# Performance work log

Measured on AMD Instinct MI355X. Metric: run time of the kernel, lower is better.

## Reference

```python
import jax, jax.numpy as jnp
import numpy as np

NK, NQ, D = 8192, 8192, 64


def setup_inputs() -> dict:
    key = jax.random.key(0)
    k1, k2, k3, k4 = jax.random.split(key, 4)
    K = jax.random.normal(k1, (NK, D), dtype=jnp.float32)
    V = jax.random.normal(k2, (NK, D), dtype=jnp.float32)
    Q = jax.random.normal(k3, (NQ, D), dtype=jnp.float32)
    m = jax.random.normal(k4, (NQ, NK), dtype=jnp.float32)  # additive edge/mask data
    return {"K": K, "V": V, "Q": Q, "m": m}


def reference(K, V, Q, m):
    d = Q.shape[-1]
    scale = 1.0 / jnp.sqrt(jnp.asarray(d, dtype=Q.dtype))
    # affinity: scaled dot product + additive m (edge information / mask)
    QKt = jnp.einsum("qd,kd->qk", Q, K) * scale + m  # [NQ, NK]
    # norm: softmax over keys
    QKt_n = jax.nn.softmax(QKt, axis=-1)
    return QKt_n @ V  # [NQ, D]
```

## Files before the change

### kernel.cpp

```cpp
#include <hip/hip_runtime.h>

#define NKK 8192
#define NQQ 8192
#define DDIM 64

typedef __attribute__((ext_vector_type(8))) short short8;
typedef __attribute__((ext_vector_type(4))) float f32x4;

static __device__ __forceinline__ unsigned short f2b(float x) {
  unsigned int u = __builtin_bit_cast(unsigned int, x);
  unsigned int r = (u + 0x7fffu + ((u >> 16) & 1u)) >> 16;
  return (unsigned short)r;
}

__global__ __launch_bounds__(256) void prep_kernel(
    const float* __restrict__ K, const float* __restrict__ V, const float* __restrict__ Q,
    unsigned short* __restrict__ Kb, unsigned short* __restrict__ Qb, unsigned short* __restrict__ Vtb) {
  __shared__ unsigned short vt[64][72];
  const int b = blockIdx.x, t = threadIdx.x;
  const size_t base = (size_t)b * 4096;
#pragma unroll
  for (int i = 0; i < 4; ++i) {
    size_t idx = base + (size_t)i * 1024 + (size_t)t * 4;
    float4 kv = *(const float4*)(K + idx);
    float4 qv = *(const float4*)(Q + idx);
    ushort4 ko, qo;
    ko.x = f2b(kv.x); ko.y = f2b(kv.y); ko.z = f2b(kv.z); ko.w = f2b(kv.w);
    qo.x = f2b(qv.x); qo.y = f2b(qv.y); qo.z = f2b(qv.z); qo.w = f2b(qv.w);
    *(ushort4*)(Kb + idx) = ko;
    *(ushort4*)(Qb + idx) = qo;
  }
  const int r0 = b * 64;
#pragma unroll
  for (int i = 0; i < 4; ++i) {
    int kl = (t >> 4) + i * 16;
    int c4 = (t & 15) * 4;
    float4 v = *(const float4*)(V + (size_t)(r0 + kl) * 64 + c4);
    vt[c4 + 0][kl] = f2b(v.x);
    vt[c4 + 1][kl] = f2b(v.y);
    vt[c4 + 2][kl] = f2b(v.z);
    vt[c4 + 3][kl] = f2b(v.w);
  }
  __syncthreads();
  {
    int d = t >> 2, kc = (t & 3) * 16;
    uint4 a0 = *(const uint4*)(&vt[d][kc]);
    uint4 a1 = *(const uint4*)(&vt[d][kc + 8]);
    *(uint4*)(Vtb + (size_t)d * NKK + r0 + kc) = a0;
    *(uint4*)(Vtb + (size_t)d * NKK + r0 + kc + 8) = a1;
  }
}

__global__ __launch_bounds__(512, 2) void attn_kernel(
    const float* __restrict__ mg, const unsigned short* __restrict__ Kb,
    const unsigned short* __restrict__ Qb, const unsigned short* __restrict__ Vtb,
    float* __restrict__ out) {
  __shared__ unsigned short Pl[8][32 * 40];
  __shared__ float accslot[4][8][4][64];
  __shared__ float lslot[4][8][4];

  const int tid = threadIdx.x;
  const int wid = tid >> 6;
  const int lane = tid & 63;
  const int c = lane & 15;
  const int g = lane >> 4;
  const int q0 = blockIdx.x * 32;

  const float LOG2E = 1.4426950408889634f;
  const float C1 = 0.125f * LOG2E;
  const float MM = -8.0f * LOG2E;

  short8 qf[4];
#pragma unroll
  for (int qs = 0; qs < 2; ++qs)
#pragma unroll
    for (int dh = 0; dh < 2; ++dh)
      qf[qs * 2 + dh] = __builtin_bit_cast(
          short8, *(const uint4*)(Qb + (size_t)(q0 + qs * 16 + c) * 64 + dh * 32 + 8 * g));

  f32x4 acc[2][4];
#pragma unroll
  for (int a = 0; a < 2; ++a)
#pragma unroll
    for (int b2 = 0; b2 < 4; ++b2) acc[a][b2] = f32x4{0.f, 0.f, 0.f, 0.f};
  float lsum[8];
#pragma unroll
  for (int n = 0; n < 8; ++n) lsum[n] = 0.f;

  unsigned short* Pw = &Pl[wid][0];
  const unsigned short* Pr = &Pl[wid][c * 40 + 8 * g];
  const unsigned int mbase = (unsigned int)(q0 + 4 * g) * (unsigned int)NKK + (unsigned int)c;

  float mA[16], mB[16];
  short8 kA[4], kB[4], vA[4], vB[4];

  auto loadM = [&](int t, float (&mb)[16]) {
    const unsigned int toff = (unsigned int)((wid + 8 * t) * 32);
    const float* mp = mg + mbase + toff;
#pragma unroll
    for (int qs = 0; qs < 2; ++qs)
#pragma unroll
      for (int ks = 0; ks < 2; ++ks)
#pragma unroll
        for (int i = 0; i < 4; ++i)
          mb[qs * 8 + ks * 4 + i] = mp[(unsigned int)(qs * 16 + i) * NKK + ks * 16];
  };

  auto loadKV = [&](int t, short8 (&kf)[4], short8 (&vf)[4]) {
    const int k0 = (wid + 8 * t) * 32;
#pragma unroll
    for (int ks = 0; ks < 2; ++ks)
#pragma unroll
      for (int dh = 0; dh < 2; ++dh)
        kf[ks * 2 + dh] = __builtin_bit_cast(
            short8, *(const uint4*)(Kb + (size_t)(k0 + ks * 16 + c) * 64 + dh * 32 + 8 * g));
#pragma unroll
    for (int dt = 0; dt < 4; ++dt)
      vf[dt] = __builtin_bit_cast(
          short8, *(const uint4*)(Vtb + (size_t)(dt * 16 + c) * NKK + k0 + 8 * g));
  };

  auto compute = [&](const float (&mb)[16], const short8 (&kf)[4], const short8 (&vf)[4]) {
    f32x4 s[2][2];
#pragma unroll
    for (int qs = 0; qs < 2; ++qs)
#pragma unroll
      for (int ks = 0; ks < 2; ++ks) {
        f32x4 z = f32x4{0.f, 0.f, 0.f, 0.f};
        z = __builtin_amdgcn_mfma_f32_16x16x32_bf16(qf[qs * 2 + 0], kf[ks * 2 + 0], z, 0, 0, 0);
        z = __builtin_amdgcn_mfma_f32_16x16x32_bf16(qf[qs * 2 + 1], kf[ks * 2 + 1], z, 0, 0, 0);
        s[qs][ks] = z;
      }
#pragma unroll
    for (int qs = 0; qs < 2; ++qs)
#pragma unroll
      for (int ks = 0; ks < 2; ++ks)
#pragma unroll
        for (int i = 0; i < 4; ++i) {
          float e = __builtin_fmaf(s[qs][ks][i], C1,
                                   __builtin_fmaf(mb[qs * 8 + ks * 4 + i], LOG2E, MM));
          float p = __builtin_amdgcn_exp2f(e);
          lsum[qs * 4 + i] += p;
          Pw[(qs * 16 + 4 * g + i) * 40 + ks * 16 + c] = f2b(p);
        }
    short8 pa[2];
#pragma unroll
    for (int qs = 0; qs < 2; ++qs)
      pa[qs] = __builtin_bit_cast(short8, *(const uint4*)(Pr + qs * 640));
#pragma unroll
    for (int qs = 0; qs < 2; ++qs)
#pragma unroll
      for (int dt = 0; dt < 4; ++dt)
        acc[qs][dt] = __builtin_amdgcn_mfma_f32_16x16x32_bf16(pa[qs], vf[dt], acc[qs][dt], 0, 0, 0);
  };

  loadM(0, mA);
  loadKV(0, kA, vA);
  for (int t = 0; t < 32; t += 2) {
    loadM(t + 1, mB);
    loadKV(t + 1, kB, vB);
    compute(mA, kA, vA);
    if (t + 2 < 32) {
      loadM(t + 2, mA);
      loadKV(t + 2, kA, vA);
    }
    compute(mB, kB, vB);
  }

#pragma unroll
  for (int n = 0; n < 8; ++n) {
    float v = lsum[n];
    v += __shfl_xor(v, 1);
    v += __shfl_xor(v, 2);
    v += __shfl_xor(v, 4);
    v += __shfl_xor(v, 8);
    lsum[n] = v;
  }

  auto writeSlot = [&](int slot) {
#pragma unroll
    for (int qs = 0; qs < 2; ++qs)
#pragma unroll
      for (int dt = 0; dt < 4; ++dt)
#pragma unroll
        for (int i = 0; i < 4; ++i) accslot[slot][qs * 4 + dt][i][lane] = acc[qs][dt][i];
    if (c == 0) {
#pragma unroll
      for (int n = 0; n < 8; ++n) lslot[slot][n][g] = lsum[n];
    }
  };
  auto addSlot = [&](int slot) {
#pragma unroll
    for (int qs = 0; qs < 2; ++qs)
#pragma unroll
      for (int dt = 0; dt < 4; ++dt)
#pragma unroll
        for (int i = 0; i < 4; ++i) acc[qs][dt][i] += accslot[slot][qs * 4 + dt][i][lane];
#pragma unroll
    for (int n = 0; n < 8; ++n) lsum[n] += lslot[slot][n][g];
  };

  if (wid >= 4) writeSlot(wid - 4);
  __syncthreads();
  if (wid < 4) addSlot(wid);
  __syncthreads();
  if (wid == 2 || wid == 3) writeSlot(wid - 2);
  __syncthreads();
  if (wid < 2) addSlot(wid);
  __syncthreads();
  if (wid == 1) writeSlot(0);
  __syncthreads();
  if (wid == 0) {
    addSlot(0);
#pragma unroll
    for (int qs = 0; qs < 2; ++qs)
#pragma unroll
      for (int i = 0; i < 4; ++i) {
        float rl = 1.0f / lsum[qs * 4 + i];
        int q = q0 + qs * 16 + 4 * g + i;
#pragma unroll
        for (int dt = 0; dt < 4; ++dt)
          out[(size_t)q * 64 + dt * 16 + c] = acc[qs][dt][i] * rl;
      }
  }
}

extern "C" void kernel_launch(void* const* d_in, const int* in_sizes, int n_in,
                              void* d_out, int out_size, void* d_ws, size_t ws_size,
                              hipStream_t stream) {
  (void)in_sizes; (void)n_in; (void)out_size; (void)ws_size;
  const float* K = (const float*)d_in[0];
  const float* V = (const float*)d_in[1];
  const float* Q = (const float*)d_in[2];
  const float* mg = (const float*)d_in[3];
  float* out = (float*)d_out;

  unsigned short* Kb = (unsigned short*)d_ws;
  unsigned short* Qb = Kb + (size_t)NKK * DDIM;
  unsigned short* Vtb = Qb + (size_t)NQQ * DDIM;

  prep_kernel<<<128, 256, 0, stream>>>(K, V, Q, Kb, Qb, Vtb);
  attn_kernel<<<256, 512, 0, stream>>>(mg, Kb, Qb, Vtb, out);
}
```

Baseline: 395.7 us.

## Transpose QK MFMA so each lane reads contiguous mask rows, halve query tile

```diff
diff --git a/kernel.cpp b/kernel.cpp
--- a/kernel.cpp
+++ b/kernel.cpp
@@ -6,11 +6,15 @@
 
 typedef __attribute__((ext_vector_type(8))) short short8;
 typedef __attribute__((ext_vector_type(4))) float f32x4;
+typedef __attribute__((ext_vector_type(2))) unsigned int u32x2;
 
 static __device__ __forceinline__ unsigned short f2b(float x) {
   unsigned int u = __builtin_bit_cast(unsigned int, x);
   unsigned int r = (u + 0x7fffu + ((u >> 16) & 1u)) >> 16;
   return (unsigned short)r;
+}
+static __device__ __forceinline__ unsigned int pk2(float a, float b) {
+  return (unsigned int)f2b(a) | ((unsigned int)f2b(b) << 16);
 }
 
 __global__ __launch_bounds__(256) void prep_kernel(
@@ -51,153 +55,109 @@
   }
 }
 
-__global__ __launch_bounds__(512, 2) void attn_kernel(
+__global__ __launch_bounds__(512, 4) void attn_kernel(
     const float* __restrict__ mg, const unsigned short* __restrict__ Kb,
     const unsigned short* __restrict__ Qb, const unsigned short* __restrict__ Vtb,
     float* __restrict__ out) {
-  __shared__ unsigned short Pl[8][32 * 40];
-  __shared__ float accslot[4][8][4][64];
-  __shared__ float lslot[4][8][4];
+  __shared__ unsigned short Pl[8][16][40];
+  __shared__ float accslot[4][4][4][64];
+  __shared__ float lslot[4][64];
 
   const int tid = threadIdx.x;
   const int wid = tid >> 6;
   const int lane = tid & 63;
   const int c = lane & 15;
   const int g = lane >> 4;
-  const int q0 = blockIdx.x * 32;
+  const int q0 = blockIdx.x * 16;
 
   const float LOG2E = 1.4426950408889634f;
   const float C1 = 0.125f * LOG2E;
   const float MM = -8.0f * LOG2E;
 
-  short8 qf[4];
-#pragma unroll
-  for (int qs = 0; qs < 2; ++qs)
-#pragma unroll
-    for (int dh = 0; dh < 2; ++dh)
-      qf[qs * 2 + dh] = __builtin_bit_cast(
-          short8, *(const uint4*)(Qb + (size_t)(q0 + qs * 16 + c) * 64 + dh * 32 + 8 * g));
-
-  f32x4 acc[2][4];
-#pragma unroll
-  for (int a = 0; a < 2; ++a)
-#pragma unroll
-    for (int b2 = 0; b2 < 4; ++b2) acc[a][b2] = f32x4{0.f, 0.f, 0.f, 0.f};
-  float lsum[8];
-#pragma unroll
-  for (int n = 0; n < 8; ++n) lsum[n] = 0.f;
-
-  unsigned short* Pw = &Pl[wid][0];
-  const unsigned short* Pr = &Pl[wid][c * 40 + 8 * g];
-  const unsigned int mbase = (unsigned int)(q0 + 4 * g) * (unsigned int)NKK + (unsigned int)c;
-
-  float mA[16], mB[16];
-  short8 kA[4], kB[4], vA[4], vB[4];
-
-  auto loadM = [&](int t, float (&mb)[16]) {
-    const unsigned int toff = (unsigned int)((wid + 8 * t) * 32);
-    const float* mp = mg + mbase + toff;
-#pragma unroll
-    for (int qs = 0; qs < 2; ++qs)
-#pragma unroll
-      for (int ks = 0; ks < 2; ++ks)
-#pragma unroll
-        for (int i = 0; i < 4; ++i)
-          mb[qs * 8 + ks * 4 + i] = mp[(unsigned int)(qs * 16 + i) * NKK + ks * 16];
-  };
-
-  auto loadKV = [&](int t, short8 (&kf)[4], short8 (&vf)[4]) {
+  short8 qf[2];
+#pragma unroll
+  for (int dh = 0; dh < 2; ++dh)
+    qf[dh] = __builtin_bit_cast(
+        short8, *(const uint4*)(Qb + (size_t)(q0 + c) * 64 + dh * 32 + 8 * g));
+
+  f32x4 acc[4];
+#pragma unroll
+  for (int dt = 0; dt < 4; ++dt) acc[dt] = f32x4{0.f, 0.f, 0.f, 0.f};
+  float lsum = 0.f;
+
+  const float* mrow = mg + (size_t)(q0 + c) * NKK + 4 * g;
+
+  f32x4 mA[2], mB[2];
+
+  auto loadM = [&](int t, f32x4 (&mb)[2]) {
+    const float* p = mrow + (unsigned)((wid + 8 * t) * 32);
+    mb[0] = *(const f32x4*)(p);
+    mb[1] = *(const f32x4*)(p + 16);
+  };
+
+  auto computeTile = [&](int t, const f32x4 (&mb)[2]) {
     const int k0 = (wid + 8 * t) * 32;
-#pragma unroll
-    for (int ks = 0; ks < 2; ++ks)
+    short8 kf[4];
+#pragma unroll
+    for (int kb = 0; kb < 2; ++kb)
 #pragma unroll
       for (int dh = 0; dh < 2; ++dh)
-        kf[ks * 2 + dh] = __builtin_bit_cast(
-            short8, *(const uint4*)(Kb + (size_t)(k0 + ks * 16 + c) * 64 + dh * 32 + 8 * g));
+        kf[kb * 2 + dh] = __builtin_bit_cast(
+            short8, *(const uint4*)(Kb + (size_t)(k0 + kb * 16 + c) * 64 + dh * 32 + 8 * g));
+    short8 vf[4];
 #pragma unroll
     for (int dt = 0; dt < 4; ++dt)
       vf[dt] = __builtin_bit_cast(
           short8, *(const uint4*)(Vtb + (size_t)(dt * 16 + c) * NKK + k0 + 8 * g));
-  };
-
-  auto compute = [&](const float (&mb)[16], const short8 (&kf)[4], const short8 (&vf)[4]) {
-    f32x4 s[2][2];
-#pragma unroll
-    for (int qs = 0; qs < 2; ++qs)
-#pragma unroll
-      for (int ks = 0; ks < 2; ++ks) {
-        f32x4 z = f32x4{0.f, 0.f, 0.f, 0.f};
-        z = __builtin_amdgcn_mfma_f32_16x16x32_bf16(qf[qs * 2 + 0], kf[ks * 2 + 0], z, 0, 0, 0);
-        z = __builtin_amdgcn_mfma_f32_16x16x32_bf16(qf[qs * 2 + 1], kf[ks * 2 + 1], z, 0, 0, 0);
-        s[qs][ks] = z;
+
+#pragma unroll
+    for (int kb = 0; kb < 2; ++kb) {
+      f32x4 z = f32x4{0.f, 0.f, 0.f, 0.f};
+      z = __builtin_amdgcn_mfma_f32_16x16x32_bf16(kf[kb * 2 + 0], qf[0], z, 0, 0, 0);
+      z = __builtin_amdgcn_mfma_f32_16x16x32_bf16(kf[kb * 2 + 1], qf[1], z, 0, 0, 0);
+      float p[4];
+#pragma unroll
+      for (int i = 0; i < 4; ++i) {
+        float e = __builtin_fmaf(z[i], C1, __builtin_fmaf(mb[kb][i], LOG2E, MM));
+        p[i] = __builtin_amdgcn_exp2f(e);
+        lsum += p[i];
       }
-#pragma unroll
-    for (int qs = 0; qs < 2; ++qs)
-#pragma unroll
-      for (int ks = 0; ks < 2; ++ks)
-#pragma unroll
-        for (int i = 0; i < 4; ++i) {
-          float e = __builtin_fmaf(s[qs][ks][i], C1,
-                                   __builtin_fmaf(mb[qs * 8 + ks * 4 + i], LOG2E, MM));
-          float p = __builtin_amdgcn_exp2f(e);
-          lsum[qs * 4 + i] += p;
-          Pw[(qs * 16 + 4 * g + i) * 40 + ks * 16 + c] = f2b(p);
-        }
-    short8 pa[2];
-#pragma unroll
-    for (int qs = 0; qs < 2; ++qs)
-      pa[qs] = __builtin_bit_cast(short8, *(const uint4*)(Pr + qs * 640));
-#pragma unroll
-    for (int qs = 0; qs < 2; ++qs)
-#pragma unroll
-      for (int dt = 0; dt < 4; ++dt)
-        acc[qs][dt] = __builtin_amdgcn_mfma_f32_16x16x32_bf16(pa[qs], vf[dt], acc[qs][dt], 0, 0, 0);
+      u32x2 w;
+      w[0] = pk2(p[0], p[1]);
+      w[1] = pk2(p[2], p[3]);
+      *(u32x2*)(&Pl[wid][c][kb * 16 + 4 * g]) = w;
+    }
+    short8 pa = __builtin_bit_cast(short8, *(const uint4*)(&Pl[wid][c][8 * g]));
+#pragma unroll
+    for (int dt = 0; dt < 4; ++dt)
+      acc[dt] = __builtin_amdgcn_mfma_f32_16x16x32_bf16(pa, vf[dt], acc[dt], 0, 0, 0);
   };
 
   loadM(0, mA);
-  loadKV(0, kA, vA);
+  loadM(1, mB);
   for (int t = 0; t < 32; t += 2) {
-    loadM(t + 1, mB);
-    loadKV(t + 1, kB, vB);
-    compute(mA, kA, vA);
-    if (t + 2 < 32) {
-      loadM(t + 2, mA);
-      loadKV(t + 2, kA, vA);
-    }
-    compute(mB, kB, vB);
-  }
-
-#pragma unroll
-  for (int n = 0; n < 8; ++n) {
-    float v = lsum[n];
-    v += __shfl_xor(v, 1);
-    v += __shfl_xor(v, 2);
-    v += __shfl_xor(v, 4);
-    v += __shfl_xor(v, 8);
-    lsum[n] = v;
-  }
+    computeTile(t, mA);
+    if (t + 2 < 32) loadM(t + 2, mA);
+    computeTile(t + 1, mB);
+    if (t + 3 < 32) loadM(t + 3, mB);
+  }
+
+  lsum += __shfl_xor(lsum, 16);
+  lsum += __shfl_xor(lsum, 32);
 
   auto writeSlot = [&](int slot) {
 #pragma unroll
-    for (int qs = 0; qs < 2; ++qs)
-#pragma unroll
-      for (int dt = 0; dt < 4; ++dt)
-#pragma unroll
-        for (int i = 0; i < 4; ++i) accslot[slot][qs * 4 + dt][i][lane] = acc[qs][dt][i];
-    if (c == 0) {
-#pragma unroll
-      for (int n = 0; n < 8; ++n) lslot[slot][n][g] = lsum[n];
-    }
+    for (int dt = 0; dt < 4; ++dt)
+#pragma unroll
+      for (int i = 0; i < 4; ++i) accslot[slot][dt][i][lane] = acc[dt][i];
+    lslot[slot][lane] = lsum;
   };
   auto addSlot = [&](int slot) {
 #pragma unroll
-    for (int qs = 0; qs < 2; ++qs)
-#pragma unroll
-      for (int dt = 0; dt < 4; ++dt)
-#pragma unroll
-        for (int i = 0; i < 4; ++i) acc[qs][dt][i] += accslot[slot][qs * 4 + dt][i][lane];
-#pragma unroll
-    for (int n = 0; n < 8; ++n) lsum[n] += lslot[slot][n][g];
+    for (int dt = 0; dt < 4; ++dt)
+#pragma unroll
+      for (int i = 0; i < 4; ++i) acc[dt][i] += accslot[slot][dt][i][lane];
+    lsum += lslot[slot][lane];
   };
 
   if (wid >= 4) writeSlot(wid - 4);
@@ -213,15 +173,14 @@
   if (wid == 0) {
     addSlot(0);
 #pragma unroll
-    for (int qs = 0; qs < 2; ++qs)
-#pragma unroll
-      for (int i = 0; i < 4; ++i) {
-        float rl = 1.0f / lsum[qs * 4 + i];
-        int q = q0 + qs * 16 + 4 * g + i;
-#pragma unroll
-        for (int dt = 0; dt < 4; ++dt)
-          out[(size_t)q * 64 + dt * 16 + c] = acc[qs][dt][i] * rl;
-      }
+    for (int i = 0; i < 4; ++i) {
+      float rs = __shfl(lsum, 4 * g + i);
+      float rl = 1.0f / rs;
+      const int q = q0 + 4 * g + i;
+#pragma unroll
+      for (int dt = 0; dt < 4; ++dt)
+        out[(size_t)q * 64 + dt * 16 + c] = acc[dt][i] * rl;
+    }
   }
 }
 
@@ -240,5 +199,5 @@
   unsigned short* Vtb = Qb + (size_t)NQQ * DDIM;
 
   prep_kernel<<<128, 256, 0, stream>>>(K, V, Q, Kb, Qb, Vtb);
-  attn_kernel<<<256, 512, 0, stream>>>(mg, Kb, Qb, Vtb, out);
-}
+  attn_kernel<<<512, 512, 0, stream>>>(mg, Kb, Qb, Vtb, out);
+}
```

Measured after the change: 454.6 us. +14.9%, slower.
